# Kernel tuning notes

Measured on AMD Instinct MI355X. Metric: run time of the kernel, lower is better.

Reference implementation:

```python
import jax, jax.numpy as jnp
import numpy as np

OBS_LEN, K, B, H, MID, NC, CIN = 12, 20, 2048, 128, 256, 2, 3

def setup_inputs() -> dict:
    key = jax.random.key(0)
    ks = jax.random.split(key, 12)
    w = lambda k, s: 0.1 * jax.random.normal(k, s, dtype=jnp.float32)
    return {
        'obs_traj_rel': jax.random.normal(ks[0], (OBS_LEN, B, CIN), dtype=jnp.float32),
        'pred_lstm_hidden': jax.random.normal(ks[1], (K, B, H), dtype=jnp.float32),
        'map_w0': w(ks[2], (H, MID)), 'map_b0': jnp.zeros((MID,), jnp.float32),
        'map_w1': w(ks[3], (MID, H)), 'map_b1': jnp.zeros((H,), jnp.float32),
        'w_ih': w(ks[4], (4 * H, NC)), 'w_hh': w(ks[5], (4 * H, H)),
        'b_ih': jnp.zeros((4 * H,), jnp.float32), 'b_hh': jnp.zeros((4 * H,), jnp.float32),
        'out_w': w(ks[6], (H, NC)), 'out_b': jnp.zeros((NC,), jnp.float32),
    }

def _hard_sigmoid(x):
    # torch F.hardsigmoid: clip(x/6 + 0.5, 0, 1)
    return jnp.clip(x / 6.0 + 0.5, 0.0, 1.0)

def reference(obs_traj_rel, pred_lstm_hidden, map_w0, map_b0, map_w1, map_b1,
              w_ih, w_hh, b_ih, b_hh, out_w, out_b):
    n_coord = out_w.shape[1]
    hdim = w_hh.shape[1]
    # mapping MLP on initial hidden state: [K, B, H]
    h = jax.nn.leaky_relu(pred_lstm_hidden @ map_w0 + map_b0, negative_slope=0.01)
    h = h @ map_w1 + map_b1
    c = jnp.zeros_like(h)
    # step i uses obs[i-1] (obs[0] at i=0), sliced to first n_coord channels
    inputs = jnp.concatenate([obs_traj_rel[:1], obs_traj_rel[:-1]], axis=0)[:, :, :n_coord]  # [T, B, nc]
    bias = b_ih + b_hh

    def step(carry, x_t):
        h, c = carry  # each [K, B, H]
        # x_t [B, nc] broadcast over samples K (same gates contribution for all K)
        gx = x_t @ w_ih.T  # [B, 4H]
        gates = gx[None, :, :] + h @ w_hh.T + bias  # [K, B, 4H]
        i, f, g, o = jnp.split(gates, 4, axis=-1)
        i = _hard_sigmoid(i); f = _hard_sigmoid(f)
        g = jnp.clip(g, -1.0, 1.0); o = _hard_sigmoid(o)
        c_new = f * c + i * g
        h_new = o * jnp.clip(c_new, -1.0, 1.0)
        out = h_new @ out_w + out_b  # [K, B, nc]
        return (h_new, c_new), out

    _, outs = jax.lax.scan(step, (h, c), inputs)
    return outs  # [obs_len, K, B, n_coord]
```

## Files before the change

kernel.cpp:

```cpp
#include <hip/hip_runtime.h>
#include <stdint.h>

#define OBS_LEN 12
#define KS 20
#define BB 2048
#define HD 128
#define MIDD 256
#define NCQ 2

using f32x4  = __attribute__((ext_vector_type(4))) float;
using bf16x8 = __attribute__((ext_vector_type(8))) short;

static __device__ __forceinline__ short f2bf(float f){
  return __builtin_bit_cast(short, (__bf16)f);
}
static __device__ __forceinline__ float hsig(float x){
  return fminf(fmaxf(fmaf(x, 0.16666666666666666f, 0.5f), 0.f), 1.f);
}
static __device__ __forceinline__ float clip1(float x){
  return fminf(fmaxf(x, -1.f), 1.f);
}
static __device__ __forceinline__ f32x4 mm(bf16x8 a, bf16x8 b, f32x4 c){
  return __builtin_amdgcn_mfma_f32_16x16x32_bf16(a, b, c, 0, 0, 0);
}

__global__ __launch_bounds__(256, 1)
void CRMF_35296041239144_kernel(
    const float* __restrict__ obs,  const float* __restrict__ pred,
    const float* __restrict__ mw0,  const float* __restrict__ mb0,
    const float* __restrict__ mw1,  const float* __restrict__ mb1,
    const float* __restrict__ wih,  const float* __restrict__ whh,
    const float* __restrict__ bih,  const float* __restrict__ bhh,
    const float* __restrict__ oww,  const float* __restrict__ obb,
    float* __restrict__ outp)
{
  __shared__ __align__(16) uint16_t hbuf[2][32*HD];
  __shared__ __align__(16) uint16_t abuf[32*MIDD];
  __shared__ float2 xbuf[OBS_LEN][32];

  const int tid = threadIdx.x;
  const int w   = tid >> 6;
  const int l   = tid & 63;
  const int p   = l >> 4;
  const int ln  = l & 15;
  const int wofs = w * 32;
  const bool w3 = (w == 3);

  const int kk = blockIdx.x >> 6;
  const int b0 = (blockIdx.x & 63) * 32;

  {
    const float* src = pred + ((size_t)(kk*BB + b0))*HD;
    #pragma unroll
    for (int it=0; it<4; ++it){
      int u = tid + it*256;
      int row = u >> 5;
      int c4  = (u & 31) * 4;
      float4 v = *reinterpret_cast<const float4*>(src + row*HD + c4);
      int e = (row*HD + c4) ^ ((row&7)*8);
      uint32_t lo = (uint32_t)(uint16_t)f2bf(v.x) | ((uint32_t)(uint16_t)f2bf(v.y) << 16);
      uint32_t hi = (uint32_t)(uint16_t)f2bf(v.z) | ((uint32_t)(uint16_t)f2bf(v.w) << 16);
      *reinterpret_cast<uint32_t*>(&hbuf[0][e])   = lo;
      *reinterpret_cast<uint32_t*>(&hbuf[0][e+2]) = hi;
    }
  }
  for (int u = tid; u < OBS_LEN*32; u += 256){
    int t = u >> 5, cc = u & 31;
    int st = t ? (t-1) : 0;
    const float* pp = obs + ((size_t)st*BB + b0 + cc)*3;
    xbuf[t][cc] = make_float2(pp[0], pp[1]);
  }

  bf16x8 wfrag[8][4];
  float wihA[8], wihB[8], biasv[8];
  #pragma unroll
  for (int ct=0; ct<8; ++ct){
    int col = (ct>>1)*128 + wofs + (ct&1)*16 + ln;
    wihA[ct]  = wih[col*2];
    wihB[ct]  = wih[col*2+1];
    biasv[ct] = bih[col] + bhh[col];
    #pragma unroll
    for (int q=0; q<4; ++q){
      const float* s = whh + col*HD + q*32 + p*8;
      float4 f0 = *reinterpret_cast<const float4*>(s);
      float4 f1 = *reinterpret_cast<const float4*>(s+4);
      bf16x8 wf;
      wf[0]=f2bf(f0.x); wf[1]=f2bf(f0.y); wf[2]=f2bf(f0.z); wf[3]=f2bf(f0.w);
      wf[4]=f2bf(f1.x); wf[5]=f2bf(f1.y); wf[6]=f2bf(f1.z); wf[7]=f2bf(f1.w);
      wfrag[ct][q] = wf;
    }
  }
  bf16x8 wfragO[4];
  float ob = 0.f;
  if (w3){
    #pragma unroll
    for (int q=0; q<4; ++q){
      bf16x8 wf;
      #pragma unroll
      for (int j=0; j<8; ++j){
        int k = q*32 + p*8 + j;
        wf[j] = (ln < NCQ) ? f2bf(oww[k*NCQ + ln]) : (short)0;
      }
      wfragO[q] = wf;
    }
    if (ln < NCQ) ob = obb[ln];
  }

  __syncthreads();

  f32x4 acc1[2][4];
  #pragma unroll
  for (int ct=0; ct<4; ++ct){
    float mb = mb0[wofs*2 + ct*16 + ln];
    f32x4 v = {mb, mb, mb, mb};
    acc1[0][ct] = v; acc1[1][ct] = v;
  }
  #pragma unroll
  for (int q=0; q<4; ++q){
    bf16x8 af0 = *reinterpret_cast<const bf16x8*>(&hbuf[0][((ln   )*HD + q*32 + p*8) ^ ((ln&7)*8)]);
    bf16x8 af1 = *reinterpret_cast<const bf16x8*>(&hbuf[0][((16+ln)*HD + q*32 + p*8) ^ ((ln&7)*8)]);
    #pragma unroll
    for (int ct=0; ct<4; ++ct){
      bf16x8 wf;
      #pragma unroll
      for (int j=0; j<8; ++j)
        wf[j] = f2bf(mw0[(q*32 + p*8 + j)*MIDD + (wofs*2 + ct*16 + ln)]);
      acc1[0][ct] = mm(af0, wf, acc1[0][ct]);
      acc1[1][ct] = mm(af1, wf, acc1[1][ct]);
    }
  }
  #pragma unroll
  for (int rt=0; rt<2; ++rt)
  #pragma unroll
  for (int ct=0; ct<4; ++ct)
  #pragma unroll
  for (int r=0; r<4; ++r){
    float v = acc1[rt][ct][r];
    v = (v > 0.f) ? v : 0.01f*v;
    int row = rt*16 + p*4 + r;
    abuf[(row*MIDD + wofs*2 + ct*16 + ln) ^ ((row&7)*8)] = (uint16_t)f2bf(v);
  }
  __syncthreads();

  f32x4 acc2[2][2];
  #pragma unroll
  for (int d=0; d<2; ++d){
    float mb = mb1[wofs + d*16 + ln];
    f32x4 v = {mb, mb, mb, mb};
    acc2[0][d] = v; acc2[1][d] = v;
  }
  #pragma unroll
  for (int q=0; q<8; ++q){
    bf16x8 af0 = *reinterpret_cast<const bf16x8*>(&abuf[((ln   )*MIDD + q*32 + p*8) ^ ((ln&7)*8)]);
    bf16x8 af1 = *reinterpret_cast<const bf16x8*>(&abuf[((16+ln)*MIDD + q*32 + p*8) ^ ((ln&7)*8)]);
    #pragma unroll
    for (int d=0; d<2; ++d){
      bf16x8 wf;
      #pragma unroll
      for (int j=0; j<8; ++j)
        wf[j] = f2bf(mw1[(q*32 + p*8 + j)*HD + (wofs + d*16 + ln)]);
      acc2[0][d] = mm(af0, wf, acc2[0][d]);
      acc2[1][d] = mm(af1, wf, acc2[1][d]);
    }
  }
  float c_[2][2][4];
  #pragma unroll
  for (int rt=0; rt<2; ++rt)
  #pragma unroll
  for (int d=0; d<2; ++d)
  #pragma unroll
  for (int r=0; r<4; ++r){
    int row = rt*16 + p*4 + r;
    hbuf[0][(row*HD + wofs + d*16 + ln) ^ ((row&7)*8)] = (uint16_t)f2bf(acc2[rt][d][r]);
    c_[rt][d][r] = 0.f;
  }
  __syncthreads();

  f32x4 acc[2][8];
  f32x4 acc8[2];
  for (int t=0; t<OBS_LEN; ++t){
    const int cur = t & 1, nxt = cur ^ 1;
    #pragma unroll
    for (int rt=0; rt<2; ++rt){
      float2 xv[4];
      #pragma unroll
      for (int r=0; r<4; ++r) xv[r] = xbuf[t][rt*16 + p*4 + r];
      #pragma unroll
      for (int ct=0; ct<8; ++ct){
        f32x4 a;
        #pragma unroll
        for (int r=0; r<4; ++r)
          a[r] = fmaf(xv[r].x, wihA[ct], fmaf(xv[r].y, wihB[ct], biasv[ct]));
        acc[rt][ct] = a;
      }
    }
    if (w3){ f32x4 v = {ob,ob,ob,ob}; acc8[0] = v; acc8[1] = v; }
    #pragma unroll
    for (int q=0; q<4; ++q){
      bf16x8 af0 = *reinterpret_cast<const bf16x8*>(&hbuf[cur][((ln   )*HD + q*32 + p*8) ^ ((ln&7)*8)]);
      bf16x8 af1 = *reinterpret_cast<const bf16x8*>(&hbuf[cur][((16+ln)*HD + q*32 + p*8) ^ ((ln&7)*8)]);
      #pragma unroll
      for (int ct=0; ct<8; ++ct){
        acc[0][ct] = mm(af0, wfrag[ct][q], acc[0][ct]);
        acc[1][ct] = mm(af1, wfrag[ct][q], acc[1][ct]);
      }
      if (w3){
        acc8[0] = mm(af0, wfragO[q], acc8[0]);
        acc8[1] = mm(af1, wfragO[q], acc8[1]);
      }
    }
    if (w3 && t > 0 && ln < NCQ){
      #pragma unroll
      for (int rt=0; rt<2; ++rt)
      #pragma unroll
      for (int r=0; r<4; ++r){
        int cell = rt*16 + p*4 + r;
        outp[(((size_t)(t-1)*KS + kk)*BB + b0 + cell)*NCQ + ln] = acc8[rt][r];
      }
    }
    #pragma unroll
    for (int rt=0; rt<2; ++rt)
    #pragma unroll
    for (int d=0; d<2; ++d)
    #pragma unroll
    for (int r=0; r<4; ++r){
      float iv = hsig(acc[rt][0+d][r]);
      float fv = hsig(acc[rt][2+d][r]);
      float gv = clip1(acc[rt][4+d][r]);
      float ov = hsig(acc[rt][6+d][r]);
      float cv = fmaf(fv, c_[rt][d][r], iv*gv);
      c_[rt][d][r] = cv;
      float hv = ov * clip1(cv);
      int row = rt*16 + p*4 + r;
      hbuf[nxt][(row*HD + wofs + d*16 + ln) ^ ((row&7)*8)] = (uint16_t)f2bf(hv);
    }
    __syncthreads();
  }

  if (w3){
    f32x4 o0 = {ob,ob,ob,ob}; f32x4 o1 = o0;
    #pragma unroll
    for (int q=0; q<4; ++q){
      bf16x8 af0 = *reinterpret_cast<const bf16x8*>(&hbuf[0][((ln   )*HD + q*32 + p*8) ^ ((ln&7)*8)]);
      bf16x8 af1 = *reinterpret_cast<const bf16x8*>(&hbuf[0][((16+ln)*HD + q*32 + p*8) ^ ((ln&7)*8)]);
      o0 = mm(af0, wfragO[q], o0);
      o1 = mm(af1, wfragO[q], o1);
    }
    if (ln < NCQ){
      #pragma unroll
      for (int r=0; r<4; ++r){
        outp[(((size_t)11*KS + kk)*BB + b0 +      (p*4 + r))*NCQ + ln] = o0[r];
        outp[(((size_t)11*KS + kk)*BB + b0 + 16 + (p*4 + r))*NCQ + ln] = o1[r];
      }
    }
  }
}

extern "C" void kernel_launch(void* const* d_in, const int* in_sizes, int n_in,
                              void* d_out, int out_size, void* d_ws, size_t ws_size,
                              hipStream_t stream) {
  (void)in_sizes; (void)n_in; (void)d_ws; (void)ws_size; (void)out_size;
  CRMF_35296041239144_kernel<<<dim3(1280), dim3(256), 0, stream>>>(
      (const float*)d_in[0], (const float*)d_in[1], (const float*)d_in[2],
      (const float*)d_in[3], (const float*)d_in[4], (const float*)d_in[5],
      (const float*)d_in[6], (const float*)d_in[7], (const float*)d_in[8],
      (const float*)d_in[9], (const float*)d_in[10], (const float*)d_in[11],
      (float*)d_out);
}
```

Baseline: 196.0 us.

## Process five K-samples per block, interleaving two independent LSTM recurrences

The grid shrinks from 1280 to 256 blocks. Each block now loops over five K-samples for its batch tile, handled as two interleaved pairs plus one single. The register-resident W_hh fragments, W_ih and bias are loaded and converted to bf16 once per block instead of once per sample. Running two independent recurrences side by side gives the MFMA pipe more independent work between the per-step barriers. In exchange, accumulator register pressure roughly doubles and LDS use doubles, which risks spills or lower occupancy, and the final unpaired sample runs with no interleaving.

```diff
diff --git a/kernel.cpp b/kernel.cpp
--- a/kernel.cpp
+++ b/kernel.cpp
@@ -22,6 +22,251 @@
 }
 static __device__ __forceinline__ f32x4 mm(bf16x8 a, bf16x8 b, f32x4 c){
   return __builtin_amdgcn_mfma_f32_16x16x32_bf16(a, b, c, 0, 0, 0);
+}
+static __device__ __forceinline__ bf16x8 ldh(const uint16_t* buf, int row, int q, int p){
+  return *reinterpret_cast<const bf16x8*>(&buf[(row*HD + q*32 + p*8) ^ ((row&7)*8)]);
+}
+static __device__ __forceinline__ bf16x8 lda(const uint16_t* buf, int row, int q, int p){
+  return *reinterpret_cast<const bf16x8*>(&buf[(row*MIDD + q*32 + p*8) ^ ((row&7)*8)]);
+}
+static __device__ __forceinline__ void stage_h(const float* __restrict__ src,
+                                               uint16_t* dst, int tid){
+  #pragma unroll
+  for (int it=0; it<4; ++it){
+    int u = tid + it*256;
+    int row = u >> 5, c4 = (u & 31)*4;
+    float4 v = *reinterpret_cast<const float4*>(src + row*HD + c4);
+    int e = (row*HD + c4) ^ ((row&7)*8);
+    uint32_t lo = (uint32_t)(uint16_t)f2bf(v.x) | ((uint32_t)(uint16_t)f2bf(v.y) << 16);
+    uint32_t hi = (uint32_t)(uint16_t)f2bf(v.z) | ((uint32_t)(uint16_t)f2bf(v.w) << 16);
+    *reinterpret_cast<uint32_t*>(&dst[e])   = lo;
+    *reinterpret_cast<uint32_t*>(&dst[e+2]) = hi;
+  }
+}
+
+template<bool HASB>
+static __device__ __forceinline__ void process_pair(
+    int kkA, int kkB, int b0,
+    const float* __restrict__ pred,
+    const float* __restrict__ mw0, const float* __restrict__ mb0,
+    const float* __restrict__ mw1, const float* __restrict__ mb1,
+    float ob,
+    const bf16x8 (&wfrag)[8][4], const bf16x8 (&wfragO)[4],
+    const float (&wihA_)[8], const float (&wihB_)[8], const float (&biasv)[8],
+    uint16_t (*hA)[32*HD], uint16_t (*hB)[32*HD],
+    uint16_t* abufA, uint16_t* abufB,
+    const float2 (&xbuf)[OBS_LEN][32],
+    float* __restrict__ outp,
+    int tid, int p, int ln, int wofs, bool w3)
+{
+  __syncthreads();
+
+  stage_h(pred + ((size_t)(kkA*BB + b0))*HD, hA[0], tid);
+  if constexpr (HASB) stage_h(pred + ((size_t)(kkB*BB + b0))*HD, hB[0], tid);
+  __syncthreads();
+
+  f32x4 a1A[2][4], a1B[2][4];
+  #pragma unroll
+  for (int ct=0; ct<4; ++ct){
+    float mb = mb0[wofs*2 + ct*16 + ln];
+    f32x4 v = {mb, mb, mb, mb};
+    a1A[0][ct] = v; a1A[1][ct] = v;
+    if constexpr (HASB) { a1B[0][ct] = v; a1B[1][ct] = v; }
+  }
+  #pragma unroll
+  for (int q=0; q<4; ++q){
+    bf16x8 aA0 = ldh(hA[0], ln, q, p), aA1 = ldh(hA[0], 16+ln, q, p);
+    bf16x8 aB0, aB1;
+    if constexpr (HASB) { aB0 = ldh(hB[0], ln, q, p); aB1 = ldh(hB[0], 16+ln, q, p); }
+    #pragma unroll
+    for (int ct=0; ct<4; ++ct){
+      bf16x8 wf;
+      #pragma unroll
+      for (int j=0; j<8; ++j)
+        wf[j] = f2bf(mw0[(q*32 + p*8 + j)*MIDD + (wofs*2 + ct*16 + ln)]);
+      a1A[0][ct] = mm(aA0, wf, a1A[0][ct]);
+      a1A[1][ct] = mm(aA1, wf, a1A[1][ct]);
+      if constexpr (HASB) {
+        a1B[0][ct] = mm(aB0, wf, a1B[0][ct]);
+        a1B[1][ct] = mm(aB1, wf, a1B[1][ct]);
+      }
+    }
+  }
+  #pragma unroll
+  for (int rt=0; rt<2; ++rt)
+  #pragma unroll
+  for (int ct=0; ct<4; ++ct)
+  #pragma unroll
+  for (int r=0; r<4; ++r){
+    int row = rt*16 + p*4 + r;
+    int e = (row*MIDD + wofs*2 + ct*16 + ln) ^ ((row&7)*8);
+    float vA = a1A[rt][ct][r];
+    abufA[e] = (uint16_t)f2bf(vA > 0.f ? vA : 0.01f*vA);
+    if constexpr (HASB) {
+      float vB = a1B[rt][ct][r];
+      abufB[e] = (uint16_t)f2bf(vB > 0.f ? vB : 0.01f*vB);
+    }
+  }
+  __syncthreads();
+
+  f32x4 a2A[2][2], a2B[2][2];
+  #pragma unroll
+  for (int d=0; d<2; ++d){
+    float mb = mb1[wofs + d*16 + ln];
+    f32x4 v = {mb, mb, mb, mb};
+    a2A[0][d] = v; a2A[1][d] = v;
+    if constexpr (HASB) { a2B[0][d] = v; a2B[1][d] = v; }
+  }
+  #pragma unroll
+  for (int q=0; q<8; ++q){
+    bf16x8 aA0 = lda(abufA, ln, q, p), aA1 = lda(abufA, 16+ln, q, p);
+    bf16x8 aB0, aB1;
+    if constexpr (HASB) { aB0 = lda(abufB, ln, q, p); aB1 = lda(abufB, 16+ln, q, p); }
+    #pragma unroll
+    for (int d=0; d<2; ++d){
+      bf16x8 wf;
+      #pragma unroll
+      for (int j=0; j<8; ++j)
+        wf[j] = f2bf(mw1[(q*32 + p*8 + j)*HD + (wofs + d*16 + ln)]);
+      a2A[0][d] = mm(aA0, wf, a2A[0][d]);
+      a2A[1][d] = mm(aA1, wf, a2A[1][d]);
+      if constexpr (HASB) {
+        a2B[0][d] = mm(aB0, wf, a2B[0][d]);
+        a2B[1][d] = mm(aB1, wf, a2B[1][d]);
+      }
+    }
+  }
+  float cA[2][2][4], cB[2][2][4];
+  #pragma unroll
+  for (int rt=0; rt<2; ++rt)
+  #pragma unroll
+  for (int d=0; d<2; ++d)
+  #pragma unroll
+  for (int r=0; r<4; ++r){
+    int row = rt*16 + p*4 + r;
+    int e = (row*HD + wofs + d*16 + ln) ^ ((row&7)*8);
+    hA[0][e] = (uint16_t)f2bf(a2A[rt][d][r]);
+    cA[rt][d][r] = 0.f;
+    if constexpr (HASB) {
+      hB[0][e] = (uint16_t)f2bf(a2B[rt][d][r]);
+      cB[rt][d][r] = 0.f;
+    }
+  }
+  __syncthreads();
+
+  f32x4 accA[2][8], accB[2][8];
+  f32x4 a8A[2], a8B[2];
+  for (int t=0; t<OBS_LEN; ++t){
+    const int cur = t & 1, nxt = cur ^ 1;
+    #pragma unroll
+    for (int rt=0; rt<2; ++rt){
+      float2 xv[4];
+      #pragma unroll
+      for (int r=0; r<4; ++r) xv[r] = xbuf[t][rt*16 + p*4 + r];
+      #pragma unroll
+      for (int ct=0; ct<8; ++ct){
+        f32x4 a;
+        #pragma unroll
+        for (int r=0; r<4; ++r)
+          a[r] = fmaf(xv[r].x, wihA_[ct], fmaf(xv[r].y, wihB_[ct], biasv[ct]));
+        accA[rt][ct] = a;
+        if constexpr (HASB) accB[rt][ct] = a;
+      }
+    }
+    if (w3){
+      f32x4 v = {ob,ob,ob,ob};
+      a8A[0] = v; a8A[1] = v;
+      if constexpr (HASB) { a8B[0] = v; a8B[1] = v; }
+    }
+    #pragma unroll
+    for (int q=0; q<4; ++q){
+      bf16x8 aA0 = ldh(hA[cur], ln, q, p), aA1 = ldh(hA[cur], 16+ln, q, p);
+      bf16x8 aB0, aB1;
+      if constexpr (HASB) { aB0 = ldh(hB[cur], ln, q, p); aB1 = ldh(hB[cur], 16+ln, q, p); }
+      #pragma unroll
+      for (int ct=0; ct<8; ++ct){
+        accA[0][ct] = mm(aA0, wfrag[ct][q], accA[0][ct]);
+        accA[1][ct] = mm(aA1, wfrag[ct][q], accA[1][ct]);
+        if constexpr (HASB) {
+          accB[0][ct] = mm(aB0, wfrag[ct][q], accB[0][ct]);
+          accB[1][ct] = mm(aB1, wfrag[ct][q], accB[1][ct]);
+        }
+      }
+      if (w3){
+        a8A[0] = mm(aA0, wfragO[q], a8A[0]);
+        a8A[1] = mm(aA1, wfragO[q], a8A[1]);
+        if constexpr (HASB) {
+          a8B[0] = mm(aB0, wfragO[q], a8B[0]);
+          a8B[1] = mm(aB1, wfragO[q], a8B[1]);
+        }
+      }
+    }
+    if (w3 && t > 0 && ln < NCQ){
+      #pragma unroll
+      for (int rt=0; rt<2; ++rt)
+      #pragma unroll
+      for (int r=0; r<4; ++r){
+        int cell = rt*16 + p*4 + r;
+        outp[(((size_t)(t-1)*KS + kkA)*BB + b0 + cell)*NCQ + ln] = a8A[rt][r];
+        if constexpr (HASB)
+          outp[(((size_t)(t-1)*KS + kkB)*BB + b0 + cell)*NCQ + ln] = a8B[rt][r];
+      }
+    }
+    #pragma unroll
+    for (int rt=0; rt<2; ++rt)
+    #pragma unroll
+    for (int d=0; d<2; ++d)
+    #pragma unroll
+    for (int r=0; r<4; ++r){
+      int row = rt*16 + p*4 + r;
+      int e = (row*HD + wofs + d*16 + ln) ^ ((row&7)*8);
+      {
+        float iv = hsig(accA[rt][0+d][r]);
+        float fv = hsig(accA[rt][2+d][r]);
+        float gv = clip1(accA[rt][4+d][r]);
+        float ov = hsig(accA[rt][6+d][r]);
+        float cv = fmaf(fv, cA[rt][d][r], iv*gv);
+        cA[rt][d][r] = cv;
+        hA[nxt][e] = (uint16_t)f2bf(ov * clip1(cv));
+      }
+      if constexpr (HASB) {
+        float iv = hsig(accB[rt][0+d][r]);
+        float fv = hsig(accB[rt][2+d][r]);
+        float gv = clip1(accB[rt][4+d][r]);
+        float ov = hsig(accB[rt][6+d][r]);
+        float cv = fmaf(fv, cB[rt][d][r], iv*gv);
+        cB[rt][d][r] = cv;
+        hB[nxt][e] = (uint16_t)f2bf(ov * clip1(cv));
+      }
+    }
+    __syncthreads();
+  }
+
+  if (w3){
+    f32x4 oA0 = {ob,ob,ob,ob}, oA1 = oA0, oB0 = oA0, oB1 = oA0;
+    #pragma unroll
+    for (int q=0; q<4; ++q){
+      bf16x8 aA0 = ldh(hA[0], ln, q, p), aA1 = ldh(hA[0], 16+ln, q, p);
+      oA0 = mm(aA0, wfragO[q], oA0);
+      oA1 = mm(aA1, wfragO[q], oA1);
+      if constexpr (HASB) {
+        bf16x8 aB0 = ldh(hB[0], ln, q, p), aB1 = ldh(hB[0], 16+ln, q, p);
+        oB0 = mm(aB0, wfragO[q], oB0);
+        oB1 = mm(aB1, wfragO[q], oB1);
+      }
+    }
+    if (ln < NCQ){
+      #pragma unroll
+      for (int r=0; r<4; ++r){
+        outp[(((size_t)11*KS + kkA)*BB + b0 +      (p*4 + r))*NCQ + ln] = oA0[r];
+        outp[(((size_t)11*KS + kkA)*BB + b0 + 16 + (p*4 + r))*NCQ + ln] = oA1[r];
+        if constexpr (HASB) {
+          outp[(((size_t)11*KS + kkB)*BB + b0 +      (p*4 + r))*NCQ + ln] = oB0[r];
+          outp[(((size_t)11*KS + kkB)*BB + b0 + 16 + (p*4 + r))*NCQ + ln] = oB1[r];
+        }
+      }
+    }
+  }
 }
 
 __global__ __launch_bounds__(256, 1)
@@ -34,8 +279,10 @@
     const float* __restrict__ oww,  const float* __restrict__ obb,
     float* __restrict__ outp)
 {
-  __shared__ __align__(16) uint16_t hbuf[2][32*HD];
-  __shared__ __align__(16) uint16_t abuf[32*MIDD];
+  __shared__ __align__(16) uint16_t hbufA[2][32*HD];
+  __shared__ __align__(16) uint16_t hbufB[2][32*HD];
+  __shared__ __align__(16) uint16_t abufA[32*MIDD];
+  __shared__ __align__(16) uint16_t abufB[32*MIDD];
   __shared__ float2 xbuf[OBS_LEN][32];
 
   const int tid = threadIdx.x;
@@ -46,24 +293,10 @@
   const int wofs = w * 32;
   const bool w3 = (w == 3);
 
-  const int kk = blockIdx.x >> 6;
-  const int b0 = (blockIdx.x & 63) * 32;
-
-  {
-    const float* src = pred + ((size_t)(kk*BB + b0))*HD;
-    #pragma unroll
-    for (int it=0; it<4; ++it){
-      int u = tid + it*256;
-      int row = u >> 5;
-      int c4  = (u & 31) * 4;
-      float4 v = *reinterpret_cast<const float4*>(src + row*HD + c4);
-      int e = (row*HD + c4) ^ ((row&7)*8);
-      uint32_t lo = (uint32_t)(uint16_t)f2bf(v.x) | ((uint32_t)(uint16_t)f2bf(v.y) << 16);
-      uint32_t hi = (uint32_t)(uint16_t)f2bf(v.z) | ((uint32_t)(uint16_t)f2bf(v.w) << 16);
-      *reinterpret_cast<uint32_t*>(&hbuf[0][e])   = lo;
-      *reinterpret_cast<uint32_t*>(&hbuf[0][e+2]) = hi;
-    }
-  }
+  const int b  = blockIdx.x;
+  const int q0 = b >> 6;
+  const int b0 = (b & 63) * 32;
+
   for (int u = tid; u < OBS_LEN*32; u += 256){
     int t = u >> 5, cc = u & 31;
     int st = t ? (t-1) : 0;
@@ -72,12 +305,12 @@
   }
 
   bf16x8 wfrag[8][4];
-  float wihA[8], wihB[8], biasv[8];
+  float wihA_[8], wihB_[8], biasv[8];
   #pragma unroll
   for (int ct=0; ct<8; ++ct){
     int col = (ct>>1)*128 + wofs + (ct&1)*16 + ln;
-    wihA[ct]  = wih[col*2];
-    wihB[ct]  = wih[col*2+1];
+    wihA_[ct] = wih[col*2];
+    wihB_[ct] = wih[col*2+1];
     biasv[ct] = bih[col] + bhh[col];
     #pragma unroll
     for (int q=0; q<4; ++q){
@@ -106,161 +339,22 @@
     if (ln < NCQ) ob = obb[ln];
   }
 
-  __syncthreads();
-
-  f32x4 acc1[2][4];
-  #pragma unroll
-  for (int ct=0; ct<4; ++ct){
-    float mb = mb0[wofs*2 + ct*16 + ln];
-    f32x4 v = {mb, mb, mb, mb};
-    acc1[0][ct] = v; acc1[1][ct] = v;
-  }
-  #pragma unroll
-  for (int q=0; q<4; ++q){
-    bf16x8 af0 = *reinterpret_cast<const bf16x8*>(&hbuf[0][((ln   )*HD + q*32 + p*8) ^ ((ln&7)*8)]);
-    bf16x8 af1 = *reinterpret_cast<const bf16x8*>(&hbuf[0][((16+ln)*HD + q*32 + p*8) ^ ((ln&7)*8)]);
-    #pragma unroll
-    for (int ct=0; ct<4; ++ct){
-      bf16x8 wf;
-      #pragma unroll
-      for (int j=0; j<8; ++j)
-        wf[j] = f2bf(mw0[(q*32 + p*8 + j)*MIDD + (wofs*2 + ct*16 + ln)]);
-      acc1[0][ct] = mm(af0, wf, acc1[0][ct]);
-      acc1[1][ct] = mm(af1, wf, acc1[1][ct]);
-    }
-  }
-  #pragma unroll
-  for (int rt=0; rt<2; ++rt)
-  #pragma unroll
-  for (int ct=0; ct<4; ++ct)
-  #pragma unroll
-  for (int r=0; r<4; ++r){
-    float v = acc1[rt][ct][r];
-    v = (v > 0.f) ? v : 0.01f*v;
-    int row = rt*16 + p*4 + r;
-    abuf[(row*MIDD + wofs*2 + ct*16 + ln) ^ ((row&7)*8)] = (uint16_t)f2bf(v);
-  }
-  __syncthreads();
-
-  f32x4 acc2[2][2];
-  #pragma unroll
-  for (int d=0; d<2; ++d){
-    float mb = mb1[wofs + d*16 + ln];
-    f32x4 v = {mb, mb, mb, mb};
-    acc2[0][d] = v; acc2[1][d] = v;
-  }
-  #pragma unroll
-  for (int q=0; q<8; ++q){
-    bf16x8 af0 = *reinterpret_cast<const bf16x8*>(&abuf[((ln   )*MIDD + q*32 + p*8) ^ ((ln&7)*8)]);
-    bf16x8 af1 = *reinterpret_cast<const bf16x8*>(&abuf[((16+ln)*MIDD + q*32 + p*8) ^ ((ln&7)*8)]);
-    #pragma unroll
-    for (int d=0; d<2; ++d){
-      bf16x8 wf;
-      #pragma unroll
-      for (int j=0; j<8; ++j)
-        wf[j] = f2bf(mw1[(q*32 + p*8 + j)*HD + (wofs + d*16 + ln)]);
-      acc2[0][d] = mm(af0, wf, acc2[0][d]);
-      acc2[1][d] = mm(af1, wf, acc2[1][d]);
-    }
-  }
-  float c_[2][2][4];
-  #pragma unroll
-  for (int rt=0; rt<2; ++rt)
-  #pragma unroll
-  for (int d=0; d<2; ++d)
-  #pragma unroll
-  for (int r=0; r<4; ++r){
-    int row = rt*16 + p*4 + r;
-    hbuf[0][(row*HD + wofs + d*16 + ln) ^ ((row&7)*8)] = (uint16_t)f2bf(acc2[rt][d][r]);
-    c_[rt][d][r] = 0.f;
-  }
-  __syncthreads();
-
-  f32x4 acc[2][8];
-  f32x4 acc8[2];
-  for (int t=0; t<OBS_LEN; ++t){
-    const int cur = t & 1, nxt = cur ^ 1;
-    #pragma unroll
-    for (int rt=0; rt<2; ++rt){
-      float2 xv[4];
-      #pragma unroll
-      for (int r=0; r<4; ++r) xv[r] = xbuf[t][rt*16 + p*4 + r];
-      #pragma unroll
-      for (int ct=0; ct<8; ++ct){
-        f32x4 a;
-        #pragma unroll
-        for (int r=0; r<4; ++r)
-          a[r] = fmaf(xv[r].x, wihA[ct], fmaf(xv[r].y, wihB[ct], biasv[ct]));
-        acc[rt][ct] = a;
-      }
-    }
-    if (w3){ f32x4 v = {ob,ob,ob,ob}; acc8[0] = v; acc8[1] = v; }
-    #pragma unroll
-    for (int q=0; q<4; ++q){
-      bf16x8 af0 = *reinterpret_cast<const bf16x8*>(&hbuf[cur][((ln   )*HD + q*32 + p*8) ^ ((ln&7)*8)]);
-      bf16x8 af1 = *reinterpret_cast<const bf16x8*>(&hbuf[cur][((16+ln)*HD + q*32 + p*8) ^ ((ln&7)*8)]);
-      #pragma unroll
-      for (int ct=0; ct<8; ++ct){
-        acc[0][ct] = mm(af0, wfrag[ct][q], acc[0][ct]);
-        acc[1][ct] = mm(af1, wfrag[ct][q], acc[1][ct]);
-      }
-      if (w3){
-        acc8[0] = mm(af0, wfragO[q], acc8[0]);
-        acc8[1] = mm(af1, wfragO[q], acc8[1]);
-      }
-    }
-    if (w3 && t > 0 && ln < NCQ){
-      #pragma unroll
-      for (int rt=0; rt<2; ++rt)
-      #pragma unroll
-      for (int r=0; r<4; ++r){
-        int cell = rt*16 + p*4 + r;
-        outp[(((size_t)(t-1)*KS + kk)*BB + b0 + cell)*NCQ + ln] = acc8[rt][r];
-      }
-    }
-    #pragma unroll
-    for (int rt=0; rt<2; ++rt)
-    #pragma unroll
-    for (int d=0; d<2; ++d)
-    #pragma unroll
-    for (int r=0; r<4; ++r){
-      float iv = hsig(acc[rt][0+d][r]);
-      float fv = hsig(acc[rt][2+d][r]);
-      float gv = clip1(acc[rt][4+d][r]);
-      float ov = hsig(acc[rt][6+d][r]);
-      float cv = fmaf(fv, c_[rt][d][r], iv*gv);
-      c_[rt][d][r] = cv;
-      float hv = ov * clip1(cv);
-      int row = rt*16 + p*4 + r;
-      hbuf[nxt][(row*HD + wofs + d*16 + ln) ^ ((row&7)*8)] = (uint16_t)f2bf(hv);
-    }
-    __syncthreads();
-  }
-
-  if (w3){
-    f32x4 o0 = {ob,ob,ob,ob}; f32x4 o1 = o0;
-    #pragma unroll
-    for (int q=0; q<4; ++q){
-      bf16x8 af0 = *reinterpret_cast<const bf16x8*>(&hbuf[0][((ln   )*HD + q*32 + p*8) ^ ((ln&7)*8)]);
-      bf16x8 af1 = *reinterpret_cast<const bf16x8*>(&hbuf[0][((16+ln)*HD + q*32 + p*8) ^ ((ln&7)*8)]);
-      o0 = mm(af0, wfragO[q], o0);
-      o1 = mm(af1, wfragO[q], o1);
-    }
-    if (ln < NCQ){
-      #pragma unroll
-      for (int r=0; r<4; ++r){
-        outp[(((size_t)11*KS + kk)*BB + b0 +      (p*4 + r))*NCQ + ln] = o0[r];
-        outp[(((size_t)11*KS + kk)*BB + b0 + 16 + (p*4 + r))*NCQ + ln] = o1[r];
-      }
-    }
-  }
+  process_pair<true >(q0,      q0 + 4,  b0, pred, mw0, mb0, mw1, mb1, ob,
+                      wfrag, wfragO, wihA_, wihB_, biasv,
+                      hbufA, hbufB, abufA, abufB, xbuf, outp, tid, p, ln, wofs, w3);
+  process_pair<true >(q0 + 8,  q0 + 12, b0, pred, mw0, mb0, mw1, mb1, ob,
+                      wfrag, wfragO, wihA_, wihB_, biasv,
+                      hbufA, hbufB, abufA, abufB, xbuf, outp, tid, p, ln, wofs, w3);
+  process_pair<false>(q0 + 16, q0 + 16, b0, pred, mw0, mb0, mw1, mb1, ob,
+                      wfrag, wfragO, wihA_, wihB_, biasv,
+                      hbufA, hbufB, abufA, abufB, xbuf, outp, tid, p, ln, wofs, w3);
 }
 
 extern "C" void kernel_launch(void* const* d_in, const int* in_sizes, int n_in,
                               void* d_out, int out_size, void* d_ws, size_t ws_size,
                               hipStream_t stream) {
   (void)in_sizes; (void)n_in; (void)d_ws; (void)ws_size; (void)out_size;
-  CRMF_35296041239144_kernel<<<dim3(1280), dim3(256), 0, stream>>>(
+  CRMF_35296041239144_kernel<<<dim3(256), dim3(256), 0, stream>>>(
       (const float*)d_in[0], (const float*)d_in[1], (const float*)d_in[2],
       (const float*)d_in[3], (const float*)d_in[4], (const float*)d_in[5],
       (const float*)d_in[6], (const float*)d_in[7], (const float*)d_in[8],
```

Result: slower. 516.0 us (+163.3%).
